# Optimization experiments

Measured on AMD Instinct MI355X. Metric: run time of the kernel, lower is better.

## Reference

```python
import jax, jax.numpy as jnp
import numpy as np

NUM_VN = 4
HIDDEN = 64
N = 1_000_000
G = 8192


def setup_inputs() -> dict:
    key = jax.random.key(0)
    ks = jax.random.split(key, 8)
    node_feat = jax.random.normal(ks[0], (N, HIDDEN), dtype=jnp.float32)
    node_pos = jax.random.normal(ks[1], (N, 3), dtype=jnp.float32)
    vn_pos = jax.random.normal(ks[2], (G, 3 * NUM_VN), dtype=jnp.float32)
    batch = jnp.sort(jax.random.randint(ks[3], (N,), 0, G, dtype=jnp.int64))
    in_dim = NUM_VN ** 2  # 16
    s1 = 1.0 / np.sqrt(in_dim)
    s2 = 1.0 / np.sqrt(HIDDEN)
    W1 = jax.random.uniform(ks[4], (HIDDEN, in_dim), jnp.float32, -s1, s1)
    b1 = jax.random.uniform(ks[5], (HIDDEN,), jnp.float32, -s1, s1)
    W2 = jax.random.uniform(ks[6], (HIDDEN, HIDDEN), jnp.float32, -s2, s2)
    b2 = jax.random.uniform(ks[7], (HIDDEN,), jnp.float32, -s2, s2)
    return {"node_feat": node_feat, "node_pos": node_pos, "vn_pos": vn_pos,
            "batch": batch, "W1": W1, "b1": b1, "W2": W2, "b2": b2}


def _safe_cdist(v):
    # v: [N, num_vn, 3]; pairwise L2 distances -> [N, num_vn, num_vn]
    diff = v[:, :, None, :] - v[:, None, :, :]
    sq = jnp.sum(diff * diff, axis=-1)
    # sqrt with zero-safe gradient on the diagonal (matches torch.cdist grad=0 there)
    pos = sq > 0
    return jnp.where(pos, jnp.sqrt(jnp.where(pos, sq, 1.0)), 0.0)


def reference(node_feat, node_pos, vn_pos, batch, W1, b1, W2, b2):
    n = node_pos.shape[0]
    # gather per-node virtual-node positions, form relative vectors [N, num_vn, 3]
    info_vec = (jnp.tile(node_pos, (1, NUM_VN)) - vn_pos[batch]).reshape(n, NUM_VN, 3)
    info_scalar = _safe_cdist(info_vec).reshape(n, NUM_VN ** 2)
    norm = jnp.linalg.norm(info_scalar, axis=1, keepdims=True)
    info_scalar = info_scalar / (norm + 0.001)
    h = jax.nn.silu(info_scalar @ W1.T + b1)
    return h @ W2.T + b2
```

## Files before the change

### kernel.cpp

```cpp
#include <hip/hip_runtime.h>

#define LOG2E 1.44269504088896340736f

typedef __attribute__((ext_vector_type(8))) _Float16 half8;
typedef __attribute__((ext_vector_type(4))) float floatx4;

__global__ void prep_weights(const float* __restrict__ W1,
                             const float* __restrict__ W2,
                             float* __restrict__ W1e,
                             _Float16* __restrict__ W2h,
                             _Float16* __restrict__ W2l) {
    const int t = threadIdx.x;
    if (t < 64) {
        const int pa[6] = {0, 0, 0, 1, 1, 2};
        const int pb[6] = {1, 2, 3, 2, 3, 3};
#pragma unroll
        for (int p = 0; p < 6; ++p)
            W1e[t * 6 + p] = W1[t * 16 + pa[p] * 4 + pb[p]] + W1[t * 16 + pb[p] * 4 + pa[p]];
    }
#pragma unroll
    for (int e = t; e < 4096; e += 256) {
        const float f = W2[e];
        const _Float16 hi = (_Float16)f;
        W2h[e] = hi;
        W2l[e] = (_Float16)(f - (float)hi);
    }
}

__global__ __launch_bounds__(256, 4) void vnmlp_mfma(
    const float* __restrict__ node_pos,
    const float* __restrict__ vn_pos,
    const void*  __restrict__ batch_raw,
    const float* __restrict__ W1e,
    const _Float16* __restrict__ W2h,
    const _Float16* __restrict__ W2l,
    const float* __restrict__ b1,
    const float* __restrict__ b2,
    float*       __restrict__ out,
    int n)
{
    __shared__ _Float16 lds_h[256 * 64];

    const int t    = threadIdx.x;
    const int base = blockIdx.x * 256;
    const int i    = base + t;
    const int ic   = (i < n) ? i : (n - 1);
    const bool full = (base + 256 <= n);

    const int l  = t & 63;
    const int w  = t >> 6;
    const int lm = l & 15;
    const int q  = l >> 4;

    half8 Bh[4][2], Bl[4][2];
    floatx4 bv4[4];
#pragma unroll
    for (int c = 0; c < 4; ++c) {
#pragma unroll
        for (int ks = 0; ks < 2; ++ks) {
            const int off = (c * 16 + lm) * 64 + ks * 32 + q * 8;
            Bh[c][ks] = *(const half8*)(W2h + off);
            Bl[c][ks] = *(const half8*)(W2l + off);
        }
        bv4[c] = *(const floatx4*)(b2 + c * 16 + q * 4);
    }

    const int* b32 = (const int*)batch_raw;
    const int probe = b32[(n / 2) | 1] | b32[(n / 4) | 1] | b32[((n / 4) * 3) | 1];
    long long bi;
    if (probe == 0) bi = ((const long long*)batch_raw)[ic];
    else            bi = (long long)b32[ic];

    const float px = node_pos[3 * ic + 0];
    const float py = node_pos[3 * ic + 1];
    const float pz = node_pos[3 * ic + 2];

    const float4* vp4 = (const float4*)(vn_pos + 12 * bi);
    const float4 v0 = vp4[0], v1 = vp4[1], v2 = vp4[2];
    const float vx[4] = {px - v0.x, px - v0.w, px - v1.z, px - v2.y};
    const float vy[4] = {py - v0.y, py - v1.x, py - v1.w, py - v2.z};
    const float vz[4] = {pz - v0.z, pz - v1.y, pz - v2.x, pz - v2.w};

    float dn[6];
    float ss = 0.0f;
    {
        int p = 0;
#pragma unroll
        for (int a = 0; a < 4; ++a) {
#pragma unroll
            for (int k = a + 1; k < 4; ++k) {
                const float dx = vx[a] - vx[k];
                const float dy = vy[a] - vy[k];
                const float dz = vz[a] - vz[k];
                const float sq = dx * dx + dy * dy + dz * dz;
                dn[p++] = __builtin_amdgcn_sqrtf(sq);
                ss += sq;
            }
        }
    }
    ss *= 2.0f;
    const float inv = __builtin_amdgcn_rcpf(__builtin_amdgcn_sqrtf(ss) + 0.001f);
#pragma unroll
    for (int p = 0; p < 6; ++p) dn[p] *= inv;

#pragma unroll
    for (int c = 0; c < 8; ++c) {
        half8 v;
#pragma unroll
        for (int jj = 0; jj < 8; ++jj) {
            const int j = c * 8 + jj;
            float acc = b1[j];
#pragma unroll
            for (int p = 0; p < 6; ++p)
                acc = fmaf(dn[p], W1e[j * 6 + p], acc);
            const float e = __builtin_amdgcn_exp2f(-LOG2E * acc);
            v[jj] = (_Float16)(acc * __builtin_amdgcn_rcpf(1.0f + e));
        }
        *(half8*)&lds_h[t * 64 + ((c ^ (t & 7)) * 8)] = v;
    }

    __asm__ volatile("s_waitcnt lgkmcnt(0)" ::: "memory");

#pragma unroll 1
    for (int s = 0; s < 4; ++s) {
        const int nn = w * 64 + s * 16 + lm;
        half8 Ah[2];
#pragma unroll
        for (int ks = 0; ks < 2; ++ks) {
            const int kc = ks * 4 + q;
            Ah[ks] = *(const half8*)&lds_h[nn * 64 + ((kc ^ (nn & 7)) * 8)];
        }
        const int node = base + nn;
        const bool ok = full || (node < n);
        floatx4* orow = (floatx4*)(out + (size_t)node * 64);
#pragma unroll
        for (int c = 0; c < 4; ++c) {
            floatx4 acc = bv4[c];
#pragma unroll
            for (int ks = 0; ks < 2; ++ks) {
                acc = __builtin_amdgcn_mfma_f32_16x16x32_f16(Bh[c][ks], Ah[ks], acc, 0, 0, 0);
                acc = __builtin_amdgcn_mfma_f32_16x16x32_f16(Bl[c][ks], Ah[ks], acc, 0, 0, 0);
            }
            if (ok)
                orow[c * 4 + q] = acc;
        }
    }
}

__global__ __launch_bounds__(256) void vnmlp_fallback(
    const float* __restrict__ node_pos, const float* __restrict__ vn_pos,
    const void* __restrict__ batch_raw, const float* __restrict__ W1,
    const float* __restrict__ b1, const float* __restrict__ W2,
    const float* __restrict__ b2, float* __restrict__ out, int n)
{
    __shared__ float lds[256 * 36];
    const int t = threadIdx.x;
    const int base = blockIdx.x * 256;
    const int i = base + t;
    const bool valid = (i < n);

    float h[64];
    if (valid) {
        const int* b32 = (const int*)batch_raw;
        const int probe = b32[(n / 2) | 1] | b32[(n / 4) | 1] | b32[((n / 4) * 3) | 1];
        long long bi;
        if (probe == 0) bi = ((const long long*)batch_raw)[i];
        else            bi = (long long)b32[i];
        const float px = node_pos[3 * i], py = node_pos[3 * i + 1], pz = node_pos[3 * i + 2];
        const float* vp = vn_pos + 12 * bi;
        float vx[4], vy[4], vz[4];
#pragma unroll
        for (int k = 0; k < 4; ++k) {
            vx[k] = px - vp[3 * k]; vy[k] = py - vp[3 * k + 1]; vz[k] = pz - vp[3 * k + 2];
        }
        float dn[6]; float ss = 0.0f; int p = 0;
#pragma unroll
        for (int a = 0; a < 4; ++a)
#pragma unroll
            for (int k = a + 1; k < 4; ++k) {
                const float dx = vx[a] - vx[k], dy = vy[a] - vy[k], dz = vz[a] - vz[k];
                const float sq = dx * dx + dy * dy + dz * dz;
                dn[p++] = __builtin_amdgcn_sqrtf(sq); ss += sq;
            }
        ss *= 2.0f;
        const float inv = __builtin_amdgcn_rcpf(__builtin_amdgcn_sqrtf(ss) + 0.001f);
#pragma unroll
        for (int qq = 0; qq < 6; ++qq) dn[qq] *= inv;
        const int pa[6] = {0, 0, 0, 1, 1, 2}, pb[6] = {1, 2, 3, 2, 3, 3};
#pragma unroll
        for (int j = 0; j < 64; ++j) {
            float acc = b1[j];
#pragma unroll
            for (int qq = 0; qq < 6; ++qq)
                acc = fmaf(dn[qq], W1[j * 16 + pa[qq] * 4 + pb[qq]] + W1[j * 16 + pb[qq] * 4 + pa[qq]], acc);
            const float e = __builtin_amdgcn_exp2f(-LOG2E * acc);
            h[j] = acc * __builtin_amdgcn_rcpf(1.0f + e);
        }
    }
    float4* o4 = (float4*)out;
#pragma unroll 1
    for (int half = 0; half < 2; ++half) {
        if (half) __syncthreads();
        if (valid) {
#pragma unroll 1
            for (int j4 = 0; j4 < 8; ++j4) {
                const int j0 = half * 32 + j4 * 4;
                float a0 = b2[j0], a1 = b2[j0 + 1], a2 = b2[j0 + 2], a3 = b2[j0 + 3];
#pragma unroll
                for (int k = 0; k < 64; ++k) {
                    const float hk = h[k];
                    a0 = fmaf(hk, W2[(j0 + 0) * 64 + k], a0);
                    a1 = fmaf(hk, W2[(j0 + 1) * 64 + k], a1);
                    a2 = fmaf(hk, W2[(j0 + 2) * 64 + k], a2);
                    a3 = fmaf(hk, W2[(j0 + 3) * 64 + k], a3);
                }
                *(float4*)&lds[t * 36 + j4 * 4] = make_float4(a0, a1, a2, a3);
            }
        }
        __syncthreads();
#pragma unroll
        for (int r = 0; r < 8; ++r) {
            const int g = r * 256 + t, node = g >> 3, sub = g & 7;
            if (base + node < n)
                o4[(size_t)(base + node) * 16 + half * 8 + sub] = *(const float4*)&lds[node * 36 + sub * 4];
        }
    }
}

extern "C" void kernel_launch(void* const* d_in, const int* in_sizes, int n_in,
                              void* d_out, int out_size, void* d_ws, size_t ws_size,
                              hipStream_t stream) {
    const float* node_pos = (const float*)d_in[1];
    const float* vn_pos   = (const float*)d_in[2];
    const void*  batch    = d_in[3];
    const float* W1       = (const float*)d_in[4];
    const float* b1       = (const float*)d_in[5];
    const float* W2       = (const float*)d_in[6];
    const float* b2       = (const float*)d_in[7];
    float* out = (float*)d_out;

    const int n = in_sizes[1] / 3;
    const int blocks = (n + 255) / 256;

    const size_t WS_NEED = 1536 + 8192 + 8192;
    if (ws_size >= WS_NEED) {
        float*    W1e = (float*)d_ws;
        _Float16* W2h = (_Float16*)((char*)d_ws + 1536);
        _Float16* W2l = (_Float16*)((char*)d_ws + 1536 + 8192);
        hipLaunchKernelGGL(prep_weights, dim3(1), dim3(256), 0, stream, W1, W2, W1e, W2h, W2l);
        hipLaunchKernelGGL(vnmlp_mfma, dim3(blocks), dim3(256), 0, stream,
                           node_pos, vn_pos, batch, W1e, W2h, W2l, b1, b2, out, n);
    } else {
        hipLaunchKernelGGL(vnmlp_fallback, dim3(blocks), dim3(256), 0, stream,
                           node_pos, vn_pos, batch, W1, b1, W2, b2, out, n);
    }
}
```

Before: 428.4 us.

## Fuse weight prep into main kernel and reorder MFMA loop to cut registers

```diff
diff --git a/kernel.cpp b/kernel.cpp
--- a/kernel.cpp
+++ b/kernel.cpp
@@ -5,36 +5,13 @@
 typedef __attribute__((ext_vector_type(8))) _Float16 half8;
 typedef __attribute__((ext_vector_type(4))) float floatx4;
 
-__global__ void prep_weights(const float* __restrict__ W1,
-                             const float* __restrict__ W2,
-                             float* __restrict__ W1e,
-                             _Float16* __restrict__ W2h,
-                             _Float16* __restrict__ W2l) {
-    const int t = threadIdx.x;
-    if (t < 64) {
-        const int pa[6] = {0, 0, 0, 1, 1, 2};
-        const int pb[6] = {1, 2, 3, 2, 3, 3};
-#pragma unroll
-        for (int p = 0; p < 6; ++p)
-            W1e[t * 6 + p] = W1[t * 16 + pa[p] * 4 + pb[p]] + W1[t * 16 + pb[p] * 4 + pa[p]];
-    }
-#pragma unroll
-    for (int e = t; e < 4096; e += 256) {
-        const float f = W2[e];
-        const _Float16 hi = (_Float16)f;
-        W2h[e] = hi;
-        W2l[e] = (_Float16)(f - (float)hi);
-    }
-}
-
-__global__ __launch_bounds__(256, 4) void vnmlp_mfma(
+__global__ __launch_bounds__(256, 5) void vnmlp_mfma(
     const float* __restrict__ node_pos,
     const float* __restrict__ vn_pos,
     const void*  __restrict__ batch_raw,
-    const float* __restrict__ W1e,
-    const _Float16* __restrict__ W2h,
-    const _Float16* __restrict__ W2l,
+    const float* __restrict__ W1,
     const float* __restrict__ b1,
+    const float* __restrict__ W2,
     const float* __restrict__ b2,
     float*       __restrict__ out,
     int n)
@@ -51,19 +28,6 @@
     const int w  = t >> 6;
     const int lm = l & 15;
     const int q  = l >> 4;
-
-    half8 Bh[4][2], Bl[4][2];
-    floatx4 bv4[4];
-#pragma unroll
-    for (int c = 0; c < 4; ++c) {
-#pragma unroll
-        for (int ks = 0; ks < 2; ++ks) {
-            const int off = (c * 16 + lm) * 64 + ks * 32 + q * 8;
-            Bh[c][ks] = *(const half8*)(W2h + off);
-            Bl[c][ks] = *(const half8*)(W2l + off);
-        }
-        bv4[c] = *(const floatx4*)(b2 + c * 16 + q * 4);
-    }
 
     const int* b32 = (const int*)batch_raw;
     const int probe = b32[(n / 2) | 1] | b32[(n / 4) | 1] | b32[((n / 4) * 3) | 1];
@@ -103,6 +67,8 @@
 #pragma unroll
     for (int p = 0; p < 6; ++p) dn[p] *= inv;
 
+    const int pa[6] = {0, 0, 0, 1, 1, 2};
+    const int pb[6] = {1, 2, 3, 2, 3, 3};
 #pragma unroll
     for (int c = 0; c < 8; ++c) {
         half8 v;
@@ -111,8 +77,10 @@
             const int j = c * 8 + jj;
             float acc = b1[j];
 #pragma unroll
-            for (int p = 0; p < 6; ++p)
-                acc = fmaf(dn[p], W1e[j * 6 + p], acc);
+            for (int p = 0; p < 6; ++p) {
+                const float we = W1[j * 16 + pa[p] * 4 + pb[p]] + W1[j * 16 + pb[p] * 4 + pa[p]];
+                acc = fmaf(dn[p], we, acc);
+            }
             const float e = __builtin_amdgcn_exp2f(-LOG2E * acc);
             v[jj] = (_Float16)(acc * __builtin_amdgcn_rcpf(1.0f + e));
         }
@@ -121,108 +89,48 @@
 
     __asm__ volatile("s_waitcnt lgkmcnt(0)" ::: "memory");
 
-#pragma unroll 1
+    half8 Ah[4][2];
+#pragma unroll
     for (int s = 0; s < 4; ++s) {
         const int nn = w * 64 + s * 16 + lm;
-        half8 Ah[2];
 #pragma unroll
         for (int ks = 0; ks < 2; ++ks) {
             const int kc = ks * 4 + q;
-            Ah[ks] = *(const half8*)&lds_h[nn * 64 + ((kc ^ (nn & 7)) * 8)];
+            Ah[s][ks] = *(const half8*)&lds_h[nn * 64 + ((kc ^ (nn & 7)) * 8)];
         }
-        const int node = base + nn;
-        const bool ok = full || (node < n);
-        floatx4* orow = (floatx4*)(out + (size_t)node * 64);
+    }
+
+#pragma unroll 1
+    for (int c = 0; c < 4; ++c) {
+        half8 Bh[2], Bl[2];
 #pragma unroll
-        for (int c = 0; c < 4; ++c) {
-            floatx4 acc = bv4[c];
+        for (int ks = 0; ks < 2; ++ks) {
+            const float* wrow = W2 + (c * 16 + lm) * 64 + ks * 32 + q * 8;
+            const floatx4 f0 = *(const floatx4*)(wrow);
+            const floatx4 f1 = *(const floatx4*)(wrow + 4);
+#pragma unroll
+            for (int e = 0; e < 4; ++e) {
+                const _Float16 h0 = (_Float16)f0[e];
+                Bh[ks][e] = h0;
+                Bl[ks][e] = (_Float16)(f0[e] - (float)h0);
+                const _Float16 h1 = (_Float16)f1[e];
+                Bh[ks][4 + e] = h1;
+                Bl[ks][4 + e] = (_Float16)(f1[e] - (float)h1);
+            }
+        }
+        const floatx4 bv = *(const floatx4*)(b2 + c * 16 + q * 4);
+
+#pragma unroll
+        for (int s = 0; s < 4; ++s) {
+            floatx4 acc = bv;
 #pragma unroll
             for (int ks = 0; ks < 2; ++ks) {
-                acc = __builtin_amdgcn_mfma_f32_16x16x32_f16(Bh[c][ks], Ah[ks], acc, 0, 0, 0);
-                acc = __builtin_amdgcn_mfma_f32_16x16x32_f16(Bl[c][ks], Ah[ks], acc, 0, 0, 0);
+                acc = __builtin_amdgcn_mfma_f32_16x16x32_f16(Bh[ks], Ah[s][ks], acc, 0, 0, 0);
+                acc = __builtin_amdgcn_mfma_f32_16x16x32_f16(Bl[ks], Ah[s][ks], acc, 0, 0, 0);
             }
-            if (ok)
-                orow[c * 4 + q] = acc;
-        }
-    }
-}
-
-__global__ __launch_bounds__(256) void vnmlp_fallback(
-    const float* __restrict__ node_pos, const float* __restrict__ vn_pos,
-    const void* __restrict__ batch_raw, const float* __restrict__ W1,
-    const float* __restrict__ b1, const float* __restrict__ W2,
-    const float* __restrict__ b2, float* __restrict__ out, int n)
-{
-    __shared__ float lds[256 * 36];
-    const int t = threadIdx.x;
-    const int base = blockIdx.x * 256;
-    const int i = base + t;
-    const bool valid = (i < n);
-
-    float h[64];
-    if (valid) {
-        const int* b32 = (const int*)batch_raw;
-        const int probe = b32[(n / 2) | 1] | b32[(n / 4) | 1] | b32[((n / 4) * 3) | 1];
-        long long bi;
-        if (probe == 0) bi = ((const long long*)batch_raw)[i];
-        else            bi = (long long)b32[i];
-        const float px = node_pos[3 * i], py = node_pos[3 * i + 1], pz = node_pos[3 * i + 2];
-        const float* vp = vn_pos + 12 * bi;
-        float vx[4], vy[4], vz[4];
-#pragma unroll
-        for (int k = 0; k < 4; ++k) {
-            vx[k] = px - vp[3 * k]; vy[k] = py - vp[3 * k + 1]; vz[k] = pz - vp[3 * k + 2];
-        }
-        float dn[6]; float ss = 0.0f; int p = 0;
-#pragma unroll
-        for (int a = 0; a < 4; ++a)
-#pragma unroll
-            for (int k = a + 1; k < 4; ++k) {
-                const float dx = vx[a] - vx[k], dy = vy[a] - vy[k], dz = vz[a] - vz[k];
-                const float sq = dx * dx + dy * dy + dz * dz;
-                dn[p++] = __builtin_amdgcn_sqrtf(sq); ss += sq;
-            }
-        ss *= 2.0f;
-        const float inv = __builtin_amdgcn_rcpf(__builtin_amdgcn_sqrtf(ss) + 0.001f);
-#pragma unroll
-        for (int qq = 0; qq < 6; ++qq) dn[qq] *= inv;
-        const int pa[6] = {0, 0, 0, 1, 1, 2}, pb[6] = {1, 2, 3, 2, 3, 3};
-#pragma unroll
-        for (int j = 0; j < 64; ++j) {
-            float acc = b1[j];
-#pragma unroll
-            for (int qq = 0; qq < 6; ++qq)
-                acc = fmaf(dn[qq], W1[j * 16 + pa[qq] * 4 + pb[qq]] + W1[j * 16 + pb[qq] * 4 + pa[qq]], acc);
-            const float e = __builtin_amdgcn_exp2f(-LOG2E * acc);
-            h[j] = acc * __builtin_amdgcn_rcpf(1.0f + e);
-        }
-    }
-    float4* o4 = (float4*)out;
-#pragma unroll 1
-    for (int half = 0; half < 2; ++half) {
-        if (half) __syncthreads();
-        if (valid) {
-#pragma unroll 1
-            for (int j4 = 0; j4 < 8; ++j4) {
-                const int j0 = half * 32 + j4 * 4;
-                float a0 = b2[j0], a1 = b2[j0 + 1], a2 = b2[j0 + 2], a3 = b2[j0 + 3];
-#pragma unroll
-                for (int k = 0; k < 64; ++k) {
-                    const float hk = h[k];
-                    a0 = fmaf(hk, W2[(j0 + 0) * 64 + k], a0);
-                    a1 = fmaf(hk, W2[(j0 + 1) * 64 + k], a1);
-                    a2 = fmaf(hk, W2[(j0 + 2) * 64 + k], a2);
-                    a3 = fmaf(hk, W2[(j0 + 3) * 64 + k], a3);
-                }
-                *(float4*)&lds[t * 36 + j4 * 4] = make_float4(a0, a1, a2, a3);
-            }
-        }
-        __syncthreads();
-#pragma unroll
-        for (int r = 0; r < 8; ++r) {
-            const int g = r * 256 + t, node = g >> 3, sub = g & 7;
-            if (base + node < n)
-                o4[(size_t)(base + node) * 16 + half * 8 + sub] = *(const float4*)&lds[node * 36 + sub * 4];
+            const int node = base + w * 64 + s * 16 + lm;
+            if (full || node < n)
+                *(floatx4*)(out + (size_t)node * 64 + c * 16 + q * 4) = acc;
         }
     }
 }
@@ -242,16 +150,6 @@
     const int n = in_sizes[1] / 3;
     const int blocks = (n + 255) / 256;
 
-    const size_t WS_NEED = 1536 + 8192 + 8192;
-    if (ws_size >= WS_NEED) {
-        float*    W1e = (float*)d_ws;
-        _Float16* W2h = (_Float16*)((char*)d_ws + 1536);
-        _Float16* W2l = (_Float16*)((char*)d_ws + 1536 + 8192);
-        hipLaunchKernelGGL(prep_weights, dim3(1), dim3(256), 0, stream, W1, W2, W1e, W2h, W2l);
-        hipLaunchKernelGGL(vnmlp_mfma, dim3(blocks), dim3(256), 0, stream,
-                           node_pos, vn_pos, batch, W1e, W2h, W2l, b1, b2, out, n);
-    } else {
-        hipLaunchKernelGGL(vnmlp_fallback, dim3(blocks), dim3(256), 0, stream,
-                           node_pos, vn_pos, batch, W1, b1, W2, b2, out, n);
-    }
+    hipLaunchKernelGGL(vnmlp_mfma, dim3(blocks), dim3(256), 0, stream,
+                       node_pos, vn_pos, batch, W1, b1, W2, b2, out, n);
 }
```

Measured after the change: 467.5 us. +9.1%, slower.

## Stage MFMA output tiles through swizzled LDS for coalesced row stores

Applied to the files above, without the earlier changes.

```diff
diff --git a/kernel.cpp b/kernel.cpp
--- a/kernel.cpp
+++ b/kernel.cpp
@@ -121,28 +121,46 @@
 
     __asm__ volatile("s_waitcnt lgkmcnt(0)" ::: "memory");
 
+    char* wbytes = (char*)lds_h + w * 8192;
+
 #pragma unroll 1
-    for (int s = 0; s < 4; ++s) {
-        const int nn = w * 64 + s * 16 + lm;
-        half8 Ah[2];
-#pragma unroll
-        for (int ks = 0; ks < 2; ++ks) {
-            const int kc = ks * 4 + q;
-            Ah[ks] = *(const half8*)&lds_h[nn * 64 + ((kc ^ (nn & 7)) * 8)];
-        }
-        const int node = base + nn;
-        const bool ok = full || (node < n);
-        floatx4* orow = (floatx4*)(out + (size_t)node * 64);
-#pragma unroll
-        for (int c = 0; c < 4; ++c) {
-            floatx4 acc = bv4[c];
+    for (int sp = 0; sp < 2; ++sp) {
+        half8 Ah[2][2];
+#pragma unroll
+        for (int ss = 0; ss < 2; ++ss) {
+            const int nn = w * 64 + (sp * 2 + ss) * 16 + lm;
 #pragma unroll
             for (int ks = 0; ks < 2; ++ks) {
-                acc = __builtin_amdgcn_mfma_f32_16x16x32_f16(Bh[c][ks], Ah[ks], acc, 0, 0, 0);
-                acc = __builtin_amdgcn_mfma_f32_16x16x32_f16(Bl[c][ks], Ah[ks], acc, 0, 0, 0);
-            }
-            if (ok)
-                orow[c * 4 + q] = acc;
+                const int kc = ks * 4 + q;
+                Ah[ss][ks] = *(const half8*)&lds_h[nn * 64 + ((kc ^ (nn & 7)) * 8)];
+            }
+        }
+
+#pragma unroll
+        for (int ss = 0; ss < 2; ++ss) {
+            const int s = sp * 2 + ss;
+#pragma unroll
+            for (int c = 0; c < 4; ++c) {
+                floatx4 acc = bv4[c];
+#pragma unroll
+                for (int ks = 0; ks < 2; ++ks) {
+                    acc = __builtin_amdgcn_mfma_f32_16x16x32_f16(Bh[c][ks], Ah[ss][ks], acc, 0, 0, 0);
+                    acc = __builtin_amdgcn_mfma_f32_16x16x32_f16(Bl[c][ks], Ah[ss][ks], acc, 0, 0, 0);
+                }
+                const int sb = (lm * 256 + c * 64 + q * 16) ^ ((lm & 7) << 4);
+                *(floatx4*)(wbytes + sb) = acc;
+            }
+            const int row0 = base + w * 64 + s * 16;
+            float* oreg = out + (size_t)row0 * 64;
+#pragma unroll
+            for (int r = 0; r < 4; ++r) {
+                const int g = r * 64 + l;
+                const int row_l = g >> 4;
+                const int rb = (g * 16) ^ ((row_l & 7) << 4);
+                const floatx4 v = *(const floatx4*)(wbytes + rb);
+                if (full || (row0 + row_l) < n)
+                    *(floatx4*)(oreg + g * 4) = v;
+            }
         }
     }
 }
```

Measured after the change: 412.8 us. 3.6% less time.
